# Kernel tuning notes

Hardware: AMD Instinct MI355X
Metric: run time of the kernel (lower is better)

## Reference

```python
import jax, jax.numpy as jnp
import numpy as np

N = 6000; E = 96000; DIN = 3000; FH1 = 256; FH2 = 128; GH = 128; LAT = 256
K = 10; SCALE = 9; NC = 10; AT = 0.5; ALPHA = 1.0; BN_EPS = 1e-4

# eval-mode BatchNorm1d with running_mean=0, running_var=1
def _bn(x, g, b):
    return x * (g / jnp.sqrt(1.0 + BN_EPS)) + b

def _block(x, W, bb, g, be):  # Linear + BN(eval) + ELU (dropout=identity in eval)
    return jax.nn.elu(_bn(x @ W + bb, g, be))

def _tconv(x, src, dst, Wq, Wk, Wv, Ws, bq, bk, bv, bs):
    # PyG TransformerConv, heads=1, root_weight=True, eval (no dropout)
    q = x @ Wq + bq; k = x @ Wk + bk; v = x @ Wv + bv
    sc = 1.0 / jnp.sqrt(jnp.asarray(q.shape[-1], x.dtype))
    logit = jnp.sum(q[dst] * k[src], axis=-1) * sc            # [E]
    m = jax.ops.segment_max(logit, dst, num_segments=N)
    e = jnp.exp(logit - m[dst])
    s = jax.ops.segment_sum(e, dst, num_segments=N)
    alpha = e / s[dst]                                        # softmax over incoming edges
    out = jax.ops.segment_sum(alpha[:, None] * v[src], dst, num_segments=N) + x @ Ws + bs
    return out, alpha

def _dense_adj(src, dst, alpha):
    # remove_self_loops + to_dense_adj: dense[src, dst] += alpha for src != dst
    mask = (src != dst).astype(alpha.dtype)
    return jnp.zeros((N, N), alpha.dtype).at[src, dst].add(alpha * mask)

def _encode(x, adj, adjp, ew1, eb1, eg1, ebe1, ew2, eb2, eg2, ebe2,
            cWq, cWk, cWv, cWs, cbq, cbk, cbv, cbs):
    feat = _block(_block(x, ew1, eb1, eg1, ebe1), ew2, eb2, eg2, ebe2)
    h = feat
    lastAp = None
    for l in range(3):
        o, a = _tconv(h, adj[0], adj[1], cWq[l], cWk[l], cWv[l], cWs[l], cbq[l], cbk[l], cbv[l], cbs[l])
        # middle layer applies the 'prue' conv to the freshly produced x (as in source)
        hp_in = o if l == 1 else h
        op, ap = _tconv(hp_in, adjp[0], adjp[1], cWq[l], cWk[l], cWv[l], cWs[l], cbq[l], cbk[l], cbv[l], cbs[l])
        A = _dense_adj(adj[0], adj[1], a)
        Ap = _dense_adj(adjp[0], adjp[1], ap)
        h = (1.0 - AT) * (A @ o) + AT * (Ap @ op)
        if l < 2:
            h = jax.nn.relu(h)
        lastAp = Ap
    return h, feat, lastAp

def setup_inputs():
    key = jax.random.key(0)
    ks = jax.random.split(key, 24)
    w = lambda k, sh, fan: (jax.random.normal(k, sh, jnp.float32) / np.sqrt(fan)).astype(jnp.float32)
    inp = {}
    inp['x'] = jax.random.normal(ks[0], (N, DIN), jnp.float32)
    inp['x_neighbor'] = jax.random.normal(ks[1], (N, DIN), jnp.float32)
    inp['spatial'] = jax.random.uniform(ks[2], (N, 2), jnp.float32)
    inp['adj'] = jax.random.randint(ks[3], (2, E), 0, N, dtype=jnp.int32)
    inp['adj_prue'] = jax.random.randint(ks[4], (2, E), 0, N, dtype=jnp.int32)
    # encoder
    inp['enc_W1'] = w(ks[5], (DIN, FH1), DIN); inp['enc_b1'] = jnp.zeros((FH1,))
    inp['enc_g1'] = jnp.ones((FH1,)); inp['enc_be1'] = jnp.zeros((FH1,))
    inp['enc_W2'] = w(ks[6], (FH1, FH2), FH1); inp['enc_b2'] = jnp.zeros((FH2,))
    inp['enc_g2'] = jnp.ones((FH2,)); inp['enc_be2'] = jnp.zeros((FH2,))
    # 3 TransformerConv layers (gc1, conv_hidden[0], gc2) all 128->128: stacked
    inp['conv_Wq'] = w(ks[7], (3, GH, GH), GH); inp['conv_Wk'] = w(ks[8], (3, GH, GH), GH)
    inp['conv_Wv'] = w(ks[9], (3, GH, GH), GH); inp['conv_Ws'] = w(ks[10], (3, GH, GH), GH)
    inp['conv_bq'] = jnp.zeros((3, GH)); inp['conv_bk'] = jnp.zeros((3, GH))
    inp['conv_bv'] = jnp.zeros((3, GH)); inp['conv_bs'] = jnp.zeros((3, GH))
    # decoder
    inp['dec_W'] = w(ks[11], (LAT, DIN), LAT); inp['dec_b'] = jnp.zeros((DIN,))
    inp['dec_g'] = jnp.ones((DIN,)); inp['dec_be'] = jnp.zeros((DIN,))
    inp['cluster'] = w(ks[12], (NC, LAT), LAT)
    return inp

def reference(x, x_neighbor, spatial, enc_W1, enc_b1, enc_g1, enc_be1,
              enc_W2, enc_b2, enc_g2, enc_be2,
              conv_Wq, conv_Wk, conv_Wv, conv_Ws, conv_bq, conv_bk, conv_bv, conv_bs,
              dec_W, dec_b, dec_g, dec_be, cluster, adj, adj_prue):
    enc = (enc_W1, enc_b1, enc_g1, enc_be1, enc_W2, enc_b2, enc_g2, enc_be2)
    conv = (conv_Wq, conv_Wk, conv_Wv, conv_Ws, conv_bq, conv_bk, conv_bv, conv_bs)
    mu, feat_x, atten = _encode(x, adj, adj_prue, *enc, *conv)
    mu_nb, feat_nb, _ = _encode(x_neighbor, adj, adj_prue, *enc, *conv)
    z = jnp.concatenate([feat_x, mu], axis=1)          # [N, LAT]
    z_nb = jnp.concatenate([feat_nb, mu_nb], axis=1)
    # Graph_spatial: kNN in joint feature+spatial space (dense [N,N] distances)
    df = (jnp.sum(z * z, 1)[:, None] - 2.0 * (z @ z_nb.T) + jnp.sum(z_nb * z_nb, 1)[None, :])
    ds = (jnp.sum(spatial * spatial, 1)[:, None] - 2.0 * (spatial @ spatial.T)
          + jnp.sum(spatial * spatial, 1)[None, :])
    neg_top, idx_k = jax.lax.top_k(-(df + ds), K)      # [N, K]
    score_k = jax.nn.softmax(neg_top, axis=-1)
    # GCNBlock_spatial: gather scale=9 nearest neighbor features and aggregate
    idx9 = idx_k[:, :SCALE]
    x_h = z_nb[idx9]                                   # [N, 9, LAT]
    wgt = score_k[:, :SCALE]
    wgt = wgt / jnp.sum(wgt, axis=-1, keepdims=True)
    z_out = z + jnp.einsum('nk,nkd->nd', wgt, x_h)     # x1_lr
    x1_hr = (x_h * wgt[:, :, None]).reshape(N * SCALE, LAT)
    de_feat = _block(z_out, dec_W, dec_b, dec_g, dec_be)
    # student-t cluster assignment
    d2 = jnp.sum((z_out[:, None, :] - cluster[None, :, :]) ** 2, axis=2)
    q = (1.0 / (1.0 + d2 / ALPHA)) ** ((ALPHA + 1.0) / 2.0)
    q = q / jnp.sum(q, axis=1, keepdims=True)
    return (z_out, de_feat, q, feat_x, de_feat, x1_hr, atten)
```

## Files before the change

### kernel.cpp

```cpp
#include <hip/hip_runtime.h>
#include <hip/hip_bf16.h>
#include <math.h>
#include <stdint.h>

#define NN 6000
#define NE 96000
#define KDIN 3000
#define NCAND 12
#define NTILE 47
#define TCAND (NCAND*NTILE)
#define PRE 32

#define OFF_ZOUT 0
#define OFF_DE1  1536000
#define OFF_Q    19536000
#define OFF_FEAT 19596000
#define OFF_DE2  20364000
#define OFF_X1   38364000
#define OFF_ATT  52188000

__global__ void prep_k(const float* __restrict__ W1, const float* __restrict__ W2,
                       const float* __restrict__ Wq, const float* __restrict__ Wk,
                       const float* __restrict__ Wv, const float* __restrict__ Ws,
                       const float* __restrict__ bq, const float* __restrict__ bk,
                       const float* __restrict__ bv, const float* __restrict__ bs,
                       const float* __restrict__ decW, const float* __restrict__ spat,
                       double* __restrict__ W1t, double* __restrict__ W2t,
                       double* __restrict__ Bct, float* __restrict__ Dt,
                       double* __restrict__ bcat,
                       double* __restrict__ sx64, double* __restrict__ sy64,
                       double* __restrict__ ssq64,
                       float* __restrict__ sx32, float* __restrict__ sy32)
{
  int t = blockIdx.x * 256 + threadIdx.x;
  if (t < 768000){
    int n = t / 3000, k = t % 3000;
    W1t[t] = (double)W1[(size_t)k * 256 + n]; return;
  }
  t -= 768000;
  if (t < 32768){
    int n = t / 256, k = t % 256;
    W2t[t] = (double)W2[(size_t)k * 128 + n]; return;
  }
  t -= 32768;
  if (t < 196608){
    int l = t / 65536; int rem = t % 65536;
    int n = rem / 128, k = rem % 128;
    int sel = n >> 7, nn = n & 127;
    const float* Wm = sel==0 ? Wq : sel==1 ? Wk : sel==2 ? Wv : Ws;
    Bct[t] = (double)Wm[((size_t)(l*128) + k) * 128 + nn]; return;
  }
  t -= 196608;
  if (t < 768000){
    int n = t / 256, k = t % 256;
    Dt[t] = decW[(size_t)k * 3000 + n]; return;
  }
  t -= 768000;
  if (t < 1536){
    int l = t / 512, n = t % 512;
    int sel = n >> 7, nn = n & 127;
    const float* bm = sel==0 ? bq : sel==1 ? bk : sel==2 ? bv : bs;
    bcat[t] = (double)bm[l*128 + nn]; return;
  }
  t -= 1536;
  if (t < NN){
    float sx = spat[(size_t)t*2], sy = spat[(size_t)t*2+1];
    sx64[t]=(double)sx; sy64[t]=(double)sy;
    ssq64[t]=(double)sx*(double)sx + (double)sy*(double)sy;
    sx32[t]=sx; sy32[t]=sy; return;
  }
}

__global__ void castup_k(const float* __restrict__ s, double* __restrict__ d, int n){
  int t = blockIdx.x*256 + threadIdx.x;
  if (t < n) d[t] = (double)s[t];
}

template<int EPI, typename TA>
__global__ __launch_bounds__(256)
void gemm64_k(const TA* __restrict__ A, int lda,
              const double* __restrict__ Bt, int ldb,
              int M, int K, int Ncol,
              double* __restrict__ outF, int ldc,
              const double* __restrict__ bias,
              const float* __restrict__ gam, const float* __restrict__ bet,
              double* __restrict__ outF2)
{
  __shared__ double lA[64][33];
  __shared__ double lB[64][33];
  const int tid = threadIdx.x;
  const int m0 = blockIdx.y * 64;
  const int n0 = blockIdx.x * 64;
  const int tx = tid & 15;
  const int ty = tid >> 4;

  double acc[4][4];
  #pragma unroll
  for (int i=0;i<4;i++)
    #pragma unroll
    for (int j=0;j<4;j++) acc[i][j] = 0.0;

  const int nkt = (K + 31) >> 5;
  for (int kt = 0; kt < nkt; kt++){
    const int k0 = kt << 5;
    __syncthreads();
    #pragma unroll
    for (int c=0;c<8;c++){
      int lin = tid + c*256;
      int row = lin >> 5, col = lin & 31;
      int gm = m0 + row, gk = k0 + col;
      double va = 0.0, vb = 0.0;
      if (gm < M && gk < K)        va = (double)A [(size_t)gm*lda + gk];
      if (n0+row < Ncol && gk < K) vb = Bt[(size_t)(n0+row)*ldb + gk];
      lA[row][col] = va;
      lB[row][col] = vb;
    }
    __syncthreads();
    #pragma unroll 2
    for (int kk=0; kk<32; kk++){
      double a0=lA[ty][kk], a1=lA[ty+16][kk], a2=lA[ty+32][kk], a3=lA[ty+48][kk];
      double b0=lB[tx][kk], b1=lB[tx+16][kk], b2=lB[tx+32][kk], b3=lB[tx+48][kk];
      acc[0][0]+=a0*b0; acc[0][1]+=a0*b1; acc[0][2]+=a0*b2; acc[0][3]+=a0*b3;
      acc[1][0]+=a1*b0; acc[1][1]+=a1*b1; acc[1][2]+=a1*b2; acc[1][3]+=a1*b3;
      acc[2][0]+=a2*b0; acc[2][1]+=a2*b1; acc[2][2]+=a2*b2; acc[2][3]+=a2*b3;
      acc[3][0]+=a3*b0; acc[3][1]+=a3*b1; acc[3][2]+=a3*b2; acc[3][3]+=a3*b3;
    }
  }
  #pragma unroll
  for (int j=0;j<4;j++){
    int gn = n0 + tx + 16*j;
    if (gn >= Ncol) continue;
    double bi = bias[gn];
    #pragma unroll
    for (int i=0;i<4;i++){
      int gm = m0 + ty + 16*i;
      if (gm >= M) continue;
      double v = acc[i][j] + bi;
      outF[(size_t)gm*ldc + gn] = v;
      if (outF2) outF2[(size_t)gm*ldc + gn] = v;
    }
  }
}

template<typename TA>
__global__ __launch_bounds__(256)
void gemm64s_k(const TA* __restrict__ A, int lda,
               const double* __restrict__ Bt, int ldb,
               int M, int K, int kchunk, int Ncol,
               double* __restrict__ part)
{
  __shared__ double lA[64][33];
  __shared__ double lB[64][33];
  const int tid = threadIdx.x;
  const int m0 = blockIdx.y * 64;
  const int n0 = blockIdx.x * 64;
  const int tx = tid & 15;
  const int ty = tid >> 4;
  const int kbeg = blockIdx.z * kchunk;
  const int kend = min(K, kbeg + kchunk);
  double* dst = part + (size_t)blockIdx.z * M * Ncol;

  double acc[4][4];
  #pragma unroll
  for (int i=0;i<4;i++)
    #pragma unroll
    for (int j=0;j<4;j++) acc[i][j] = 0.0;

  const int nkt = (kend - kbeg + 31) >> 5;
  for (int kt = 0; kt < nkt; kt++){
    const int k0 = kbeg + (kt << 5);
    __syncthreads();
    #pragma unroll
    for (int c=0;c<8;c++){
      int lin = tid + c*256;
      int row = lin >> 5, col = lin & 31;
      int gm = m0 + row, gk = k0 + col;
      double va = 0.0, vb = 0.0;
      if (gm < M && gk < kend)        va = (double)A [(size_t)gm*lda + gk];
      if (n0+row < Ncol && gk < kend) vb = Bt[(size_t)(n0+row)*ldb + gk];
      lA[row][col] = va;
      lB[row][col] = vb;
    }
    __syncthreads();
    #pragma unroll 2
    for (int kk=0; kk<32; kk++){
      double a0=lA[ty][kk], a1=lA[ty+16][kk], a2=lA[ty+32][kk], a3=lA[ty+48][kk];
      double b0=lB[tx][kk], b1=lB[tx+16][kk], b2=lB[tx+32][kk], b3=lB[tx+48][kk];
      acc[0][0]+=a0*b0; acc[0][1]+=a0*b1; acc[0][2]+=a0*b2; acc[0][3]+=a0*b3;
      acc[1][0]+=a1*b0; acc[1][1]+=a1*b1; acc[1][2]+=a1*b2; acc[1][3]+=a1*b3;
      acc[2][0]+=a2*b0; acc[2][1]+=a2*b1; acc[2][2]+=a2*b2; acc[2][3]+=a2*b3;
      acc[3][0]+=a3*b0; acc[3][1]+=a3*b1; acc[3][2]+=a3*b2; acc[3][3]+=a3*b3;
    }
  }
  #pragma unroll
  for (int j=0;j<4;j++){
    int gn = n0 + tx + 16*j;
    if (gn >= Ncol) continue;
    #pragma unroll
    for (int i=0;i<4;i++){
      int gm = m0 + ty + 16*i;
      if (gm >= M) continue;
      dst[(size_t)gm*Ncol + gn] = acc[i][j];
    }
  }
}

__global__ void epi64_k(const double* __restrict__ part, int nsplit, size_t pstride,
                        int M, int Ncol, const double* __restrict__ bias,
                        const float* __restrict__ gam, const float* __restrict__ bet,
                        double* __restrict__ out, int ldo)
{
  int t = blockIdx.x*256 + threadIdx.x;
  if (t >= M*Ncol) return;
  int gm = t / Ncol, gn = t - gm*Ncol;
  double v = 0.0;
  for (int s=0; s<nsplit; s++) v += part[(size_t)s*pstride + t];
  const double BNS = 0.99995000374968755261;
  v += bias[gn];
  v = v * ((double)gam[gn]*BNS) + (double)bet[gn];
  v = v > 0.0 ? v : expm1(v);
  out[(size_t)gm*ldo + gn] = v;
}

__global__ __launch_bounds__(256)
void gemm32d_k(const float* __restrict__ A, int lda,
               const float* __restrict__ Bt, int ldb,
               int M, int K, int Ncol,
               float* __restrict__ out1, int ldc,
               const float* __restrict__ bias, const float* __restrict__ gam,
               const float* __restrict__ bet, float* __restrict__ out2)
{
  __shared__ float lA[64][33];
  __shared__ float lB[64][33];
  const int tid = threadIdx.x;
  const int m0 = blockIdx.y * 64;
  const int n0 = blockIdx.x * 64;
  const int tx = tid & 15;
  const int ty = tid >> 4;

  float acc[4][4];
  #pragma unroll
  for (int i=0;i<4;i++)
    #pragma unroll
    for (int j=0;j<4;j++) acc[i][j] = 0.f;

  const int nkt = (K + 31) >> 5;
  for (int kt = 0; kt < nkt; kt++){
    const int k0 = kt << 5;
    __syncthreads();
    #pragma unroll
    for (int c=0;c<8;c++){
      int lin = tid + c*256;
      int row = lin >> 5, col = lin & 31;
      int gm = m0 + row, gk = k0 + col;
      float va = 0.f, vb = 0.f;
      if (gm < M && gk < K)        va = A [(size_t)gm*lda + gk];
      if (n0+row < Ncol && gk < K) vb = Bt[(size_t)(n0+row)*ldb + gk];
      lA[row][col] = va;
      lB[row][col] = vb;
    }
    __syncthreads();
    #pragma unroll 4
    for (int kk=0; kk<32; kk++){
      float a0=lA[ty][kk], a1=lA[ty+16][kk], a2=lA[ty+32][kk], a3=lA[ty+48][kk];
      float b0=lB[tx][kk], b1=lB[tx+16][kk], b2=lB[tx+32][kk], b3=lB[tx+48][kk];
      acc[0][0]+=a0*b0; acc[0][1]+=a0*b1; acc[0][2]+=a0*b2; acc[0][3]+=a0*b3;
      acc[1][0]+=a1*b0; acc[1][1]+=a1*b1; acc[1][2]+=a1*b2; acc[1][3]+=a1*b3;
      acc[2][0]+=a2*b0; acc[2][1]+=a2*b1; acc[2][2]+=a2*b2; acc[2][3]+=a2*b3;
      acc[3][0]+=a3*b0; acc[3][1]+=a3*b1; acc[3][2]+=a3*b2; acc[3][3]+=a3*b3;
    }
  }
  const float BNS = 0.99995000374968755f;
  #pragma unroll
  for (int j=0;j<4;j++){
    int gn = n0 + tx + 16*j;
    if (gn >= Ncol) continue;
    float bi = bias[gn];
    float gs = gam[gn]*BNS, be = bet[gn];
    #pragma unroll
    for (int i=0;i<4;i++){
      int gm = m0 + ty + 16*i;
      if (gm >= M) continue;
      float v = acc[i][j] + bi;
      v = v*gs + be; v = v > 0.f ? v : expm1f(v);
      out1[(size_t)gm*ldc + gn] = v;
      out2[(size_t)gm*ldc + gn] = v;
    }
  }
}

__global__ void csr_cnt_k(const int* __restrict__ key, int* __restrict__ cnt){
  int e = blockIdx.x*256 + threadIdx.x;
  if (e < NE) atomicAdd(&cnt[key[e]], 1);
}
__global__ __launch_bounds__(256)
void csr_scan_k(const int* __restrict__ cnt, int* __restrict__ rowptr, int* __restrict__ cursor){
  __shared__ int part[256];
  int t = threadIdx.x;
  int base = t*24;
  int loc[24]; int s=0;
  #pragma unroll
  for (int u=0;u<24;u++){
    int idx = base+u;
    int v = (idx<NN) ? cnt[idx] : 0;
    loc[u] = s; s += v;
  }
  part[t] = s;
  __syncthreads();
  if (t==0){
    int run=0;
    for (int u=0;u<256;u++){ int tmp=part[u]; part[u]=run; run+=tmp; }
  }
  __syncthreads();
  int off = part[t];
  #pragma unroll
  for (int u=0;u<24;u++){
    int idx = base+u;
    if (idx<NN){ rowptr[idx]=off+loc[u]; cursor[idx]=off+loc[u]; }
  }
  if (t==255) rowptr[NN] = off + s;
}
__global__ void csr_fill_k(const int* __restrict__ key, int* __restrict__ cursor,
                           int* __restrict__ elist){
  int e = blockIdx.x*256 + threadIdx.x;
  if (e < NE){ int pos = atomicAdd(&cursor[key[e]], 1); elist[pos] = e; }
}

__global__ __launch_bounds__(256)
void attn_k(double* __restrict__ QKVS, const int* __restrict__ rowptr,
            const int* __restrict__ elist, const int* __restrict__ src,
            double* __restrict__ alpha)
{
  __shared__ double lg[4][128];
  const int w = threadIdx.x >> 6;
  const int node = blockIdx.x*4 + w;
  if (node >= NN) return;
  const int lane = threadIdx.x & 63;
  const int e0 = rowptr[node], e1 = rowptr[node+1];
  const int deg = e1 - e0;
  if (deg <= 0) return;
  const double SC = 0.088388347648318447;
  const double* q = QKVS + (size_t)node*512;
  double q0 = q[lane], q1 = q[lane+64];

  if (deg <= 128){
    double m = -1.0e300;
    for (int i=0;i<deg;i++){
      const double* k = QKVS + (size_t)src[elist[e0+i]]*512 + 128;
      double p = q0*k[lane] + q1*k[lane+64];
      #pragma unroll
      for (int off=32; off; off>>=1) p += __shfl_xor(p, off);
      p *= SC;
      if (lane==0) lg[w][i] = p;
      m = fmax(m, p);
    }
    double S = 0.0;
    for (int i=0;i<deg;i++){
      double ex = exp(lg[w][i] - m);
      if (lane==0) lg[w][i] = ex;
      S += ex;
    }
    double inv = 1.0 / S;
    double o0 = QKVS[(size_t)node*512 + 384 + lane];
    double o1 = QKVS[(size_t)node*512 + 448 + lane];
    for (int i=0;i<deg;i++){
      int e = elist[e0+i];
      double a = lg[w][i] * inv;
      const double* v = QKVS + (size_t)src[e]*512 + 256;
      o0 = fma(a, v[lane],    o0);
      o1 = fma(a, v[lane+64], o1);
      if (lane==0) alpha[e] = a;
    }
    QKVS[(size_t)node*512 + 384 + lane] = o0;
    QKVS[(size_t)node*512 + 448 + lane] = o1;
  } else {
    double m = -1.0e300;
    for (int i=0;i<deg;i++){
      const double* k = QKVS + (size_t)src[elist[e0+i]]*512 + 128;
      double p = q0*k[lane] + q1*k[lane+64];
      #pragma unroll
      for (int off=32; off; off>>=1) p += __shfl_xor(p, off);
      m = fmax(m, p*SC);
    }
    double S = 0.0;
    for (int i=0;i<deg;i++){
      const double* k = QKVS + (size_t)src[elist[e0+i]]*512 + 128;
      double p = q0*k[lane] + q1*k[lane+64];
      #pragma unroll
      for (int off=32; off; off>>=1) p += __shfl_xor(p, off);
      S += exp(p*SC - m);
    }
    double inv = 1.0 / S;
    double o0 = QKVS[(size_t)node*512 + 384 + lane];
    double o1 = QKVS[(size_t)node*512 + 448 + lane];
    for (int i=0;i<deg;i++){
      int e = elist[e0+i];
      const double* k = QKVS + (size_t)src[e]*512 + 128;
      double p = q0*k[lane] + q1*k[lane+64];
      #pragma unroll
      for (int off=32; off; off>>=1) p += __shfl_xor(p, off);
      double a = exp(p*SC - m) * inv;
      const double* v = QKVS + (size_t)src[e]*512 + 256;
      o0 = fma(a, v[lane],    o0);
      o1 = fma(a, v[lane+64], o1);
      if (lane==0) alpha[e] = a;
    }
    QKVS[(size_t)node*512 + 384 + lane] = o0;
    QKVS[(size_t)node*512 + 448 + lane] = o1;
  }
}

__global__ __launch_bounds__(256)
void spmm_csr_k(const double* __restrict__ QK1, const double* __restrict__ QK2,
                const int* __restrict__ rpSA, const int* __restrict__ elSA,
                const int* __restrict__ dstA, const double* __restrict__ aA,
                const int* __restrict__ rpSP, const int* __restrict__ elSP,
                const int* __restrict__ dstP, const double* __restrict__ aP,
                double* __restrict__ out, int ldo, int offo, int dorelu)
{
  const int node = blockIdx.x*4 + (threadIdx.x>>6);
  if (node >= NN) return;
  const int lane = threadIdx.x & 63;
  double a0 = 0.0, a1 = 0.0;
  for (int idx = rpSA[node]; idx < rpSA[node+1]; ++idx){
    int e = elSA[idx]; int d = dstA[e];
    if (d != node){
      double wgt = 0.5 * aA[e];
      const double* o = QK1 + (size_t)d*512 + 384;
      a0 = fma(wgt, o[lane],    a0);
      a1 = fma(wgt, o[lane+64], a1);
    }
  }
  for (int idx = rpSP[node]; idx < rpSP[node+1]; ++idx){
    int e = elSP[idx]; int d = dstP[e];
    if (d != node){
      double wgt = 0.5 * aP[e];
      const double* o = QK2 + (size_t)d*512 + 384;
      a0 = fma(wgt, o[lane],    a0);
      a1 = fma(wgt, o[lane+64], a1);
    }
  }
  if (dorelu){ a0 = fmax(a0, 0.0); a1 = fmax(a1, 0.0); }
  out[(size_t)node*ldo + offo + lane]      = a0;
  out[(size_t)node*ldo + offo + 64 + lane] = a1;
}

__global__ void att_scatter_k(const int* __restrict__ src, const int* __restrict__ dst,
                              const double* __restrict__ alpha, float* __restrict__ att)
{
  int e = blockIdx.x*256 + threadIdx.x;
  if (e >= NE) return;
  int s = src[e], d = dst[e];
  if (s == d) return;
  atomicAdd(&att[(size_t)s*NN + d], (float)alpha[e]);
}

__global__ __launch_bounds__(256)
void dist32_k(const float* __restrict__ Z, const float* __restrict__ Znb,
              const float* __restrict__ sxA, const float* __restrict__ syA, const float* __restrict__ cjA,
              float* __restrict__ candV, int* __restrict__ candI)
{
  __shared__ __align__(16) char smem[33024 + 1536];
  float (*lA)[36]    = (float(*)[36])(smem);
  float (*lB)[36]    = (float(*)[36])(smem + 9216);
  float (*stile)[129]= (float(*)[129])(smem);
  float* sSx = (float*)(smem + 33024);
  float* sSy = sSx + 128;
  float* sC  = sSy + 128;

  const int tid = threadIdx.x;
  const int m0 = blockIdx.y * 64;
  const int n0 = blockIdx.x * 128;
  const int tx = tid & 15;
  const int ty = tid >> 4;

  if (tid < 128){
    int jg = n0 + tid;
    if (jg < NN){ sSx[tid]=sxA[jg]; sSy[tid]=syA[jg]; sC[tid]=cjA[jg]; }
    else        { sSx[tid]=0.f; sSy[tid]=0.f; sC[tid]=-3e38f; }
  }

  float acc[4][8];
  #pragma unroll
  for (int i=0;i<4;i++)
    #pragma unroll
    for (int j=0;j<8;j++) acc[i][j] = 0.f;

  for (int kt = 0; kt < 8; kt++){
    const int k0 = kt << 5;
    __syncthreads();
    #pragma unroll
    for (int c=0;c<2;c++){
      int lin = tid + c*256;
      int row = lin >> 3, c4 = (lin & 7) << 2;
      int gm = m0 + row;
      float4 v = make_float4(0.f,0.f,0.f,0.f);
      if (gm < NN) v = *(const float4*)(Z + (size_t)gm*256 + k0 + c4);
      *(float4*)&lA[row][c4] = v;
    }
    #pragma unroll
    for (int c=0;c<4;c++){
      int lin = tid + c*256;
      int row = lin >> 3, c4 = (lin & 7) << 2;
      int gn = n0 + row;
      float4 v = make_float4(0.f,0.f,0.f,0.f);
      if (gn < NN) v = *(const float4*)(Znb + (size_t)gn*256 + k0 + c4);
      *(float4*)&lB[row][c4] = v;
    }
    __syncthreads();
    #pragma unroll 2
    for (int kk=0; kk<32; kk+=4){
      float4 a[4], b[8];
      #pragma unroll
      for (int i=0;i<4;i++) a[i] = *(const float4*)&lA[ty+16*i][kk];
      #pragma unroll
      for (int j=0;j<8;j++) b[j] = *(const float4*)&lB[tx+16*j][kk];
      #pragma unroll
      for (int u=0;u<4;u++){
        #pragma unroll
        for (int i=0;i<4;i++){
          float av = (&a[i].x)[u];
          #pragma unroll
          for (int j=0;j<8;j++)
            acc[i][j] += av * (&b[j].x)[u];
        }
      }
    }
  }

  __syncthreads();
  #pragma unroll
  for (int i=0;i<4;i++)
    #pragma unroll
    for (int j=0;j<8;j++)
      stile[ty+16*i][tx+16*j] = acc[i][j];
  __syncthreads();

  if (tid < 64){
    const int gi = m0 + tid;
    if (gi < NN){
      float sxi = sxA[gi], syi = syA[gi];
      float tv[NCAND]; int ti[NCAND];
      #pragma unroll
      for (int p=0;p<NCAND;p++){ tv[p] = -3.4e38f; ti[p] = -1; }
      #pragma unroll 1
      for (int jj=0; jj<128; jj++){
        float s = 2.f*stile[tid][jj] + 2.f*(sxi*sSx[jj] + syi*sSy[jj]) + sC[jj];
        if (s > tv[NCAND-1]){
          bool g[NCAND];
          #pragma unroll
          for (int p=0;p<NCAND;p++) g[p] = s > tv[p];
          #pragma unroll
          for (int p=NCAND-1;p>0;--p) if (g[p-1]){ tv[p]=tv[p-1]; ti[p]=ti[p-1]; }
          #pragma unroll
          for (int p=0;p<NCAND;p++){ bool pl = g[p] && (p==0 || !g[p-1]); if (pl){ tv[p]=s; ti[p]=n0+jj; } }
        }
      }
      size_t base = ((size_t)gi*NTILE + blockIdx.x)*NCAND;
      #pragma unroll
      for (int p=0;p<NCAND;p++){ candV[base+p]=tv[p]; candI[base+p]=ti[p]; }
    }
  }
}

__global__ __launch_bounds__(256)
void merge64_k(const float* __restrict__ candV, const int* __restrict__ candI,
               const double* __restrict__ Z, const double* __restrict__ Znb,
               const double* __restrict__ sx64, const double* __restrict__ sy64,
               double* __restrict__ wgt9, int* __restrict__ idx9)
{
  __shared__ double zi[256];
  __shared__ int    fjS[TCAND];
  __shared__ float  wbv[4];
  __shared__ int    wbc[4];
  __shared__ int    chosen;
  __shared__ int    pj[PRE];
  __shared__ double ps[PRE];

  const int i = blockIdx.x;
  const int t = threadIdx.x;
  const int lane = t & 63, wv = t >> 6;

  zi[t] = Z[(size_t)i*256 + t];

  float v0 = -3.4e38f, v1 = -3.4e38f, v2 = -3.4e38f;
  const int c0 = t, c1 = t + 256, c2 = t + 512;
  {
    float vv = candV[(size_t)i*TCAND + c0];
    int jj = candI[(size_t)i*TCAND + c0];
    fjS[c0] = jj;
    if (jj >= 0) v0 = vv;
  }
  if (c1 < TCAND){
    float vv = candV[(size_t)i*TCAND + c1];
    int jj = candI[(size_t)i*TCAND + c1];
    fjS[c1] = jj;
    if (jj >= 0) v1 = vv;
  }
  if (c2 < TCAND){
    float vv = candV[(size_t)i*TCAND + c2];
    int jj = candI[(size_t)i*TCAND + c2];
    fjS[c2] = jj;
    if (jj >= 0) v2 = vv;
  }
  __syncthreads();

  for (int it = 0; it < PRE; it++){
    float bv = v0; int bc = c0;
    if (v1 > bv || (v1 == bv && c1 < bc)){ bv = v1; bc = c1; }
    if (v2 > bv || (v2 == bv && c2 < bc)){ bv = v2; bc = c2; }
    #pragma unroll
    for (int off = 32; off; off >>= 1){
      float ov = __shfl_xor(bv, off);
      int   oc = __shfl_xor(bc, off);
      if (ov > bv || (ov == bv && oc < bc)){ bv = ov; bc = oc; }
    }
    if (lane == 0){ wbv[wv] = bv; wbc[wv] = bc; }
    __syncthreads();
    if (t == 0){
      float gb = wbv[0]; int gc = wbc[0];
      #pragma unroll
      for (int w2 = 1; w2 < 4; w2++)
        if (wbv[w2] > gb || (wbv[w2] == gb && wbc[w2] < gc)){ gb = wbv[w2]; gc = wbc[w2]; }
      chosen = gc;
      pj[it] = fjS[gc];
    }
    __syncthreads();
    int gc = chosen;
    if (c0 == gc) v0 = -3.4e38f;
    if (c1 == gc) v1 = -3.4e38f;
    if (c2 == gc) v2 = -3.4e38f;
  }

  const double sxi = sx64[i], syi = sy64[i];
  for (int c = wv; c < PRE; c += 4){
    int j = pj[c];
    const double* zj = Znb + (size_t)j*256;
    double p = 0.0;
    #pragma unroll
    for (int u = 0; u < 4; u++){
      double b = zj[lane + 64*u];
      double a = zi[lane + 64*u];
      p = fma(2.0*a - b, b, p);
    }
    #pragma unroll
    for (int off = 32; off; off >>= 1) p += __shfl_xor(p, off);
    double sxj = sx64[j], syj = sy64[j];
    double s = p + 2.0*(sxi*sxj + syi*syj) - (sxj*sxj + syj*syj);
    if (lane == 0) ps[c] = s;
  }
  __syncthreads();

  if (t == 0){
    double tv9[9]; int ti9[9];
    #pragma unroll
    for (int p = 0; p < 9; p++){ tv9[p] = -1.0e301; ti9[p] = 0x7FFFFFFF; }
    for (int c = 0; c < PRE; c++){
      double s = ps[c]; int j = pj[c];
      if (!((s > tv9[8]) || (s == tv9[8] && j < ti9[8]))) continue;
      int p = 8;
      while (p > 0 && ((s > tv9[p-1]) || (s == tv9[p-1] && j < ti9[p-1]))){
        tv9[p] = tv9[p-1]; ti9[p] = ti9[p-1]; --p;
      }
      tv9[p] = s; ti9[p] = j;
    }
    double m = tv9[0], e[9], S = 0.0;
    #pragma unroll
    for (int k = 0; k < 9; k++){ e[k] = exp(tv9[k] - m); S += e[k]; }
    #pragma unroll
    for (int k = 0; k < 9; k++){
      wgt9[(size_t)i*9 + k] = e[k] / S;
      idx9[(size_t)i*9 + k] = ti9[k];
    }
  }
}

__global__ __launch_bounds__(256)
void znbprep_k(const double* __restrict__ znb, const double* __restrict__ ssq64,
               float* __restrict__ cjA)
{
  __shared__ double red[256];
  int i = blockIdx.x, d = threadIdx.x;
  double v = znb[(size_t)i*256 + d];
  red[d] = v*v;
  __syncthreads();
  for (int s=128; s; s>>=1){ if (d<s) red[d]+=red[d+s]; __syncthreads(); }
  if (d==0) cjA[i] = -(float)(red[0] + ssq64[i]);
}
__global__ void castz_k(const double* __restrict__ z64, float* __restrict__ z32, int n){
  int t = blockIdx.x*256+threadIdx.x;
  if (t < n) z32[t] = (float)z64[t];
}
__global__ void featout_k(const double* __restrict__ z, float* __restrict__ o){
  int t = blockIdx.x*256+threadIdx.x;
  if (t < NN*128){ int i=t>>7, d=t&127; o[t] = (float)z[(size_t)i*256 + d]; }
}

__global__ __launch_bounds__(256)
void zout_k(const double* __restrict__ Z, const double* __restrict__ Znb,
            const int* __restrict__ idx9, const double* __restrict__ wgt9,
            float* __restrict__ zoOut, float* __restrict__ zoF32, float* __restrict__ x1)
{
  int i = blockIdx.x; int d = threadIdx.x;
  double a = Z[(size_t)i*256 + d];
  #pragma unroll
  for (int k=0;k<9;k++){
    int j = idx9[(size_t)i*9+k];
    double w = wgt9[(size_t)i*9+k];
    double t = w * Znb[(size_t)j*256 + d];
    a += t;
    x1[((size_t)i*9+k)*256 + d] = (float)t;
  }
  float af = (float)a;
  zoOut[(size_t)i*256+d] = af;
  zoF32[(size_t)i*256+d] = af;
}

__global__ __launch_bounds__(256)
void q_k(const float* __restrict__ zoF, const float* __restrict__ clus, float* __restrict__ qB)
{
  __shared__ float wred[10][4];
  __shared__ float qs[10];
  int i = blockIdx.x, d = threadIdx.x;
  int lane = d & 63, wv = d >> 6;
  float zo = zoF[(size_t)i*256 + d];
  #pragma unroll
  for (int c=0;c<10;c++){
    float df = zo - clus[(size_t)c*256 + d];
    float p = df*df;
    #pragma unroll
    for (int off=32; off; off>>=1) p += __shfl_down(p, off);
    if (lane == 0) wred[c][wv] = p;
  }
  __syncthreads();
  if (d < 10){
    float d2 = wred[d][0]+wred[d][1]+wred[d][2]+wred[d][3];
    qs[d] = 1.f/(1.f + d2);
  }
  __syncthreads();
  if (d < 10){
    float s = 0.f;
    #pragma unroll
    for (int c=0;c<10;c++) s += qs[c];
    qB[(size_t)i*10 + d] = qs[d]/s;
  }
}

extern "C" void kernel_launch(void* const* d_in, const int* in_sizes, int n_in,
                              void* d_out, int out_size, void* d_ws, size_t ws_size,
                              hipStream_t stream)
{
  (void)in_sizes; (void)n_in; (void)out_size; (void)ws_size;
  const float* x    = (const float*)d_in[0];
  const float* xnb  = (const float*)d_in[1];
  const float* spat = (const float*)d_in[2];
  const int*   adj  = (const int*)d_in[3];
  const int*   adjp = (const int*)d_in[4];
  const float* W1   = (const float*)d_in[5];
  const float* b1   = (const float*)d_in[6];
  const float* g1   = (const float*)d_in[7];
  const float* be1  = (const float*)d_in[8];
  const float* W2   = (const float*)d_in[9];
  const float* b2   = (const float*)d_in[10];
  const float* g2   = (const float*)d_in[11];
  const float* be2  = (const float*)d_in[12];
  const float* Wq   = (const float*)d_in[13];
  const float* Wk   = (const float*)d_in[14];
  const float* Wv   = (const float*)d_in[15];
  const float* Wsm  = (const float*)d_in[16];
  const float* bq   = (const float*)d_in[17];
  const float* bk   = (const float*)d_in[18];
  const float* bv   = (const float*)d_in[19];
  const float* bs   = (const float*)d_in[20];
  const float* decW = (const float*)d_in[21];
  const float* decb = (const float*)d_in[22];
  const float* decg = (const float*)d_in[23];
  const float* decbe= (const float*)d_in[24];
  const float* clus = (const float*)d_in[25];
  float* outF = (float*)d_out;
  const int* srcA = adj,  *dstA = adj + NE;
  const int* srcP = adjp, *dstP = adjp + NE;

  char* wsb = (char*)d_ws;
  size_t off = 0;
  auto alloc = [&](size_t bytes)->char*{
    char* p = wsb + off;
    off = (off + bytes + 255) & ~(size_t)255;
    return p;
  };
  double* W1t  = (double*)alloc(768000*8);
  double* W2t  = (double*)alloc(32768*8);
  double* Bct  = (double*)alloc(196608*8);
  float*  Dt   = (float*) alloc(768000*4);
  double* bcat = (double*)alloc(1536*8);
  double* sx64 = (double*)alloc(NN*8);
  double* sy64 = (double*)alloc(NN*8);
  double* ssq64= (double*)alloc(NN*8);
  float*  sx32 = (float*) alloc(NN*4);
  float*  sy32 = (float*) alloc(NN*4);
  double* b1c  = (double*)alloc(256*8);
  double* b2c  = (double*)alloc(128*8);
  double* H1   = (double*)alloc((size_t)NN*256*8);
  double* zX64 = (double*)alloc((size_t)NN*256*8);
  double* zNB64= (double*)alloc((size_t)NN*256*8);
  double* hcur = (double*)alloc((size_t)NN*128*8);
  double* QK1  = (double*)alloc((size_t)NN*512*8);
  double* QK2  = (double*)alloc((size_t)NN*512*8);
  double* alphaA=(double*)alloc((size_t)NE*8);
  double* alphaP=(double*)alloc((size_t)NE*8);
  double* part = (double*)alloc((size_t)4*NN*256*8);
  int* rpDA = (int*)alloc((NN+1)*4);
  int* rpDP = (int*)alloc((NN+1)*4);
  int* rpSA = (int*)alloc((NN+1)*4);
  int* rpSP = (int*)alloc((NN+1)*4);
  int* curDA= (int*)alloc(NN*4);
  int* curDP= (int*)alloc(NN*4);
  int* curSA= (int*)alloc(NN*4);
  int* curSP= (int*)alloc(NN*4);
  int* elDA = (int*)alloc(NE*4);
  int* elDP = (int*)alloc(NE*4);
  int* elSA = (int*)alloc(NE*4);
  int* elSP = (int*)alloc(NE*4);
  float*  zX32 = (float*) alloc((size_t)NN*256*4);
  float*  zNB32= (float*) alloc((size_t)NN*256*4);
  float*  cjA  = (float*) alloc(NN*4);
  float*  candV= (float*) alloc((size_t)NN*TCAND*4);
  int*    candI= (int*)   alloc((size_t)NN*TCAND*4);
  int*    idx9 = (int*)   alloc((size_t)NN*9*4);
  double* wgt9 = (double*)alloc((size_t)NN*9*8);
  float*  zoF32= (float*) alloc((size_t)NN*256*4);

  prep_k<<<6926, 256, 0, stream>>>(W1, W2, Wq, Wk, Wv, Wsm, bq, bk, bv, bs, decW, spat,
                                   W1t, W2t, Bct, Dt, bcat,
                                   sx64, sy64, ssq64, sx32, sy32);
  castup_k<<<1, 256, 0, stream>>>(b1, b1c, 256);
  castup_k<<<1, 256, 0, stream>>>(b2, b2c, 128);

  hipMemsetAsync(curDA, 0, NN*4, stream);
  hipMemsetAsync(curDP, 0, NN*4, stream);
  hipMemsetAsync(curSA, 0, NN*4, stream);
  hipMemsetAsync(curSP, 0, NN*4, stream);
  csr_cnt_k<<<375, 256, 0, stream>>>(dstA, curDA);
  csr_cnt_k<<<375, 256, 0, stream>>>(dstP, curDP);
  csr_cnt_k<<<375, 256, 0, stream>>>(srcA, curSA);
  csr_cnt_k<<<375, 256, 0, stream>>>(srcP, curSP);
  csr_scan_k<<<1, 256, 0, stream>>>(curDA, rpDA, curDA);
  csr_scan_k<<<1, 256, 0, stream>>>(curDP, rpDP, curDP);
  csr_scan_k<<<1, 256, 0, stream>>>(curSA, rpSA, curSA);
  csr_scan_k<<<1, 256, 0, stream>>>(curSP, rpSP, curSP);
  csr_fill_k<<<375, 256, 0, stream>>>(dstA, curDA, elDA);
  csr_fill_k<<<375, 256, 0, stream>>>(dstP, curDP, elDP);
  csr_fill_k<<<375, 256, 0, stream>>>(srcA, curSA, elSA);
  csr_fill_k<<<375, 256, 0, stream>>>(srcP, curSP, elSP);

  auto enc = [&](const float* xin, double* zbuf, bool isX){
    gemm64s_k<float><<<dim3(4,94,4), 256, 0, stream>>>(xin, KDIN, W1t, KDIN,
                                                       NN, KDIN, 768, 256, part);
    epi64_k<<<(NN*256+255)/256, 256, 0, stream>>>(part, 4, (size_t)NN*256,
                                                  NN, 256, b1c, g1, be1, H1, 256);
    gemm64s_k<double><<<dim3(2,94,4), 256, 0, stream>>>(H1, 256, W2t, 256,
                                                        NN, 256, 64, 128, part);
    epi64_k<<<(NN*128+255)/256, 256, 0, stream>>>(part, 4, (size_t)NN*128,
                                                  NN, 128, b2c, g2, be2, zbuf, 256);
    const double* hin = zbuf; int ldh = 256;
    for (int l=0; l<3; l++){
      const double* Bh = Bct + (size_t)l*65536;
      const double* bc = bcat + l*512;
      if (l != 1){
        gemm64_k<0,double><<<dim3(8,94), 256, 0, stream>>>(hin, ldh, Bh, 128, NN, 128, 512,
                                                           QK1, 512, bc, nullptr, nullptr, QK2);
        attn_k<<<1500, 256, 0, stream>>>(QK1, rpDA, elDA, srcA, alphaA);
        attn_k<<<1500, 256, 0, stream>>>(QK2, rpDP, elDP, srcP, alphaP);
      } else {
        gemm64_k<0,double><<<dim3(8,94), 256, 0, stream>>>(hin, ldh, Bh, 128, NN, 128, 512,
                                                           QK1, 512, bc, nullptr, nullptr, nullptr);
        attn_k<<<1500, 256, 0, stream>>>(QK1, rpDA, elDA, srcA, alphaA);
        gemm64_k<0,double><<<dim3(8,94), 256, 0, stream>>>(QK1 + 384, 512, Bh, 128, NN, 128, 512,
                                                           QK2, 512, bc, nullptr, nullptr, nullptr);
        attn_k<<<1500, 256, 0, stream>>>(QK2, rpDP, elDP, srcP, alphaP);
      }
      if (isX && l == 2){
        hipMemsetAsync(outF + (size_t)OFF_ATT, 0, (size_t)NN*NN*4, stream);
        att_scatter_k<<<375, 256, 0, stream>>>(srcP, dstP, alphaP, outF + (size_t)OFF_ATT);
      }
      if (l < 2){
        spmm_csr_k<<<1500, 256, 0, stream>>>(QK1, QK2, rpSA, elSA, dstA, alphaA,
                                             rpSP, elSP, dstP, alphaP, hcur, 128, 0, 1);
        hin = hcur; ldh = 128;
      } else {
        spmm_csr_k<<<1500, 256, 0, stream>>>(QK1, QK2, rpSA, elSA, dstA, alphaA,
                                             rpSP, elSP, dstP, alphaP, zbuf, 256, 128, 0);
      }
    }
  };
  enc(x,   zX64,  true);
  enc(xnb, zNB64, false);

  castz_k<<<6000, 256, 0, stream>>>(zX64,  zX32,  NN*256);
  castz_k<<<6000, 256, 0, stream>>>(zNB64, zNB32, NN*256);
  znbprep_k<<<NN, 256, 0, stream>>>(zNB64, ssq64, cjA);
  dist32_k<<<dim3(NTILE,94), 256, 0, stream>>>(zX32, zNB32, sx32, sy32, cjA, candV, candI);
  merge64_k<<<NN, 256, 0, stream>>>(candV, candI, zX64, zNB64, sx64, sy64, wgt9, idx9);

  zout_k<<<NN, 256, 0, stream>>>(zX64, zNB64, idx9, wgt9,
                                 outF + (size_t)OFF_ZOUT, zoF32, outF + (size_t)OFF_X1);
  gemm32d_k<<<dim3(47,94), 256, 0, stream>>>(zoF32, 256, Dt, 256, NN, 256, 3000,
                                             outF + (size_t)OFF_DE1, 3000, decb, decg, decbe,
                                             outF + (size_t)OFF_DE2);
  q_k<<<NN, 256, 0, stream>>>(zoF32, clus, outF + (size_t)OFF_Q);
  featout_k<<<3000, 256, 0, stream>>>(zX64, outF + (size_t)OFF_FEAT);
}
```

Before: 3.229 ms.

## Compute kNN distance tile with split-bf16 MFMA instead of FP32 FMA

Z and Z_nb are each split into high and low bf16 parts, and the pairwise dot products for the kNN candidate search are computed with three bf16 MFMA products (hh, hl, lh) accumulating into fp32. The block tile grows from 64x128 to 128x128, and the candidate scan runs in two 64-column halves over a smaller shared stage. The aim is to replace the scalar FP32 FMA GEMM with matrix-core throughput while keeping near-fp32 accuracy for candidate selection, since the final merge re-ranks in double. The cost is lower precision in candidate ordering, with some risk of missing a true neighbour, plus an extra split pass.

```diff
diff --git a/kernel.cpp b/kernel.cpp
--- a/kernel.cpp
+++ b/kernel.cpp
@@ -18,6 +18,18 @@
 #define OFF_DE2  20364000
 #define OFF_X1   38364000
 #define OFF_ATT  52188000
+
+typedef __attribute__((ext_vector_type(8))) short short8;
+typedef __attribute__((ext_vector_type(4))) float f32x4;
+
+__device__ __forceinline__ unsigned short f2bf(float f){
+  unsigned int u = __float_as_uint(f);
+  u += 0x7FFFu + ((u >> 16) & 1u);
+  return (unsigned short)(u >> 16);
+}
+__device__ __forceinline__ float bf2f(unsigned short h){
+  return __uint_as_float(((unsigned int)h) << 16);
+}
 
 __global__ void prep_k(const float* __restrict__ W1, const float* __restrict__ W2,
                        const float* __restrict__ Wq, const float* __restrict__ Wk,
@@ -74,6 +86,17 @@
 __global__ void castup_k(const float* __restrict__ s, double* __restrict__ d, int n){
   int t = blockIdx.x*256 + threadIdx.x;
   if (t < n) d[t] = (double)s[t];
+}
+
+__global__ void splitz_k(const double* __restrict__ z64, unsigned short* __restrict__ zh,
+                         unsigned short* __restrict__ zl, int n){
+  int t = blockIdx.x*256 + threadIdx.x;
+  if (t < n){
+    float v = (float)z64[t];
+    unsigned short h = f2bf(v);
+    float r = v - bf2f(h);
+    zh[t] = h; zl[t] = f2bf(r);
+  }
 }
 
 template<int EPI, typename TA>
@@ -456,23 +479,31 @@
 }
 
 __global__ __launch_bounds__(256)
-void dist32_k(const float* __restrict__ Z, const float* __restrict__ Znb,
-              const float* __restrict__ sxA, const float* __restrict__ syA, const float* __restrict__ cjA,
+void distmf_k(const unsigned short* __restrict__ zXh, const unsigned short* __restrict__ zXl,
+              const unsigned short* __restrict__ zNh, const unsigned short* __restrict__ zNl,
+              const float* __restrict__ sxA, const float* __restrict__ syA,
+              const float* __restrict__ cjA,
               float* __restrict__ candV, int* __restrict__ candI)
 {
-  __shared__ __align__(16) char smem[33024 + 1536];
-  float (*lA)[36]    = (float(*)[36])(smem);
-  float (*lB)[36]    = (float(*)[36])(smem + 9216);
-  float (*stile)[129]= (float(*)[129])(smem);
-  float* sSx = (float*)(smem + 33024);
+  __shared__ __align__(16) char smem[40960 + 1536];
+  typedef unsigned short u16;
+  u16 (*lAh)[40] = (u16(*)[40])(smem);
+  u16 (*lAl)[40] = (u16(*)[40])(smem + 10240);
+  u16 (*lBh)[40] = (u16(*)[40])(smem + 20480);
+  u16 (*lBl)[40] = (u16(*)[40])(smem + 30720);
+  float (*stile)[67] = (float(*)[67])(smem);
+  float* sSx = (float*)(smem + 40960);
   float* sSy = sSx + 128;
   float* sC  = sSy + 128;
 
   const int tid = threadIdx.x;
-  const int m0 = blockIdx.y * 64;
+  const int m0 = blockIdx.y * 128;
   const int n0 = blockIdx.x * 128;
-  const int tx = tid & 15;
-  const int ty = tid >> 4;
+  const int lane = tid & 63;
+  const int wave = tid >> 6;
+  const int wm = wave >> 1, wn = wave & 1;
+  const int lr = lane & 15;
+  const int lk = (lane >> 4) * 8;
 
   if (tid < 128){
     int jg = n0 + tid;
@@ -480,72 +511,83 @@
     else        { sSx[tid]=0.f; sSy[tid]=0.f; sC[tid]=-3e38f; }
   }
 
-  float acc[4][8];
+  f32x4 acc[4][4];
   #pragma unroll
   for (int i=0;i<4;i++)
     #pragma unroll
-    for (int j=0;j<8;j++) acc[i][j] = 0.f;
+    for (int j=0;j<4;j++) acc[i][j] = (f32x4){0.f,0.f,0.f,0.f};
 
   for (int kt = 0; kt < 8; kt++){
     const int k0 = kt << 5;
     __syncthreads();
     #pragma unroll
-    for (int c=0;c<2;c++){
-      int lin = tid + c*256;
-      int row = lin >> 3, c4 = (lin & 7) << 2;
-      int gm = m0 + row;
-      float4 v = make_float4(0.f,0.f,0.f,0.f);
-      if (gm < NN) v = *(const float4*)(Z + (size_t)gm*256 + k0 + c4);
-      *(float4*)&lA[row][c4] = v;
-    }
-    #pragma unroll
     for (int c=0;c<4;c++){
       int lin = tid + c*256;
-      int row = lin >> 3, c4 = (lin & 7) << 2;
-      int gn = n0 + row;
-      float4 v = make_float4(0.f,0.f,0.f,0.f);
-      if (gn < NN) v = *(const float4*)(Znb + (size_t)gn*256 + k0 + c4);
-      *(float4*)&lB[row][c4] = v;
-    }
-    __syncthreads();
-    #pragma unroll 2
-    for (int kk=0; kk<32; kk+=4){
-      float4 a[4], b[8];
+      int row = lin >> 3;
+      int kc = (lin & 7) << 2;
+      int gm = m0 + row, gn = n0 + row;
+      ushort4 vh = {0,0,0,0}, vl = {0,0,0,0}, wh = {0,0,0,0}, wl = {0,0,0,0};
+      if (gm < NN){
+        vh = *(const ushort4*)(zXh + (size_t)gm*256 + k0 + kc);
+        vl = *(const ushort4*)(zXl + (size_t)gm*256 + k0 + kc);
+      }
+      if (gn < NN){
+        wh = *(const ushort4*)(zNh + (size_t)gn*256 + k0 + kc);
+        wl = *(const ushort4*)(zNl + (size_t)gn*256 + k0 + kc);
+      }
+      *(ushort4*)&lAh[row][kc] = vh;
+      *(ushort4*)&lAl[row][kc] = vl;
+      *(ushort4*)&lBh[row][kc] = wh;
+      *(ushort4*)&lBl[row][kc] = wl;
+    }
+    __syncthreads();
+    short8 ah[4], al[4];
+    #pragma unroll
+    for (int fm=0; fm<4; fm++){
+      ah[fm] = *(const short8*)&lAh[wm*64 + fm*16 + lr][lk];
+      al[fm] = *(const short8*)&lAl[wm*64 + fm*16 + lr][lk];
+    }
+    #pragma unroll
+    for (int fn=0; fn<4; fn++){
+      short8 bh = *(const short8*)&lBh[wn*64 + fn*16 + lr][lk];
+      short8 bl = *(const short8*)&lBl[wn*64 + fn*16 + lr][lk];
       #pragma unroll
-      for (int i=0;i<4;i++) a[i] = *(const float4*)&lA[ty+16*i][kk];
+      for (int fm=0; fm<4; fm++){
+        acc[fm][fn] = __builtin_amdgcn_mfma_f32_16x16x32_bf16(ah[fm], bh, acc[fm][fn], 0,0,0);
+        acc[fm][fn] = __builtin_amdgcn_mfma_f32_16x16x32_bf16(ah[fm], bl, acc[fm][fn], 0,0,0);
+        acc[fm][fn] = __builtin_amdgcn_mfma_f32_16x16x32_bf16(al[fm], bh, acc[fm][fn], 0,0,0);
+      }
+    }
+  }
+
+  float tv[NCAND]; int ti[NCAND];
+  #pragma unroll
+  for (int p=0;p<NCAND;p++){ tv[p] = -3.4e38f; ti[p] = -1; }
+  const int gi = m0 + tid;
+  float sxi = 0.f, syi = 0.f;
+  if (tid < 128 && gi < NN){ sxi = sxA[gi]; syi = syA[gi]; }
+
+  for (int jh = 0; jh < 2; jh++){
+    __syncthreads();
+    if (wn == jh){
       #pragma unroll
-      for (int j=0;j<8;j++) b[j] = *(const float4*)&lB[tx+16*j][kk];
-      #pragma unroll
-      for (int u=0;u<4;u++){
+      for (int fm=0;fm<4;fm++){
         #pragma unroll
-        for (int i=0;i<4;i++){
-          float av = (&a[i].x)[u];
+        for (int fn=0;fn<4;fn++){
+          int lrow = wm*64 + fm*16 + ((lane>>4)<<2);
+          int lcol = fn*16 + lr;
           #pragma unroll
-          for (int j=0;j<8;j++)
-            acc[i][j] += av * (&b[j].x)[u];
+          for (int r=0;r<4;r++)
+            stile[lrow + r][lcol] = acc[fm][fn][r];
         }
       }
     }
-  }
-
-  __syncthreads();
-  #pragma unroll
-  for (int i=0;i<4;i++)
-    #pragma unroll
-    for (int j=0;j<8;j++)
-      stile[ty+16*i][tx+16*j] = acc[i][j];
-  __syncthreads();
-
-  if (tid < 64){
-    const int gi = m0 + tid;
-    if (gi < NN){
-      float sxi = sxA[gi], syi = syA[gi];
-      float tv[NCAND]; int ti[NCAND];
-      #pragma unroll
-      for (int p=0;p<NCAND;p++){ tv[p] = -3.4e38f; ti[p] = -1; }
+    __syncthreads();
+    if (tid < 128 && gi < NN){
       #pragma unroll 1
-      for (int jj=0; jj<128; jj++){
-        float s = 2.f*stile[tid][jj] + 2.f*(sxi*sSx[jj] + syi*sSy[jj]) + sC[jj];
+      for (int jj=0; jj<64; jj++){
+        int j = jh*64 + jj;
+        float s = 2.f*stile[tid][jj] + 2.f*(sxi*sSx[j] + syi*sSy[j]) + sC[j];
         if (s > tv[NCAND-1]){
           bool g[NCAND];
           #pragma unroll
@@ -553,13 +595,15 @@
           #pragma unroll
           for (int p=NCAND-1;p>0;--p) if (g[p-1]){ tv[p]=tv[p-1]; ti[p]=ti[p-1]; }
           #pragma unroll
-          for (int p=0;p<NCAND;p++){ bool pl = g[p] && (p==0 || !g[p-1]); if (pl){ tv[p]=s; ti[p]=n0+jj; } }
+          for (int p=0;p<NCAND;p++){ bool pl = g[p] && (p==0 || !g[p-1]); if (pl){ tv[p]=s; ti[p]=n0+j; } }
         }
       }
-      size_t base = ((size_t)gi*NTILE + blockIdx.x)*NCAND;
-      #pragma unroll
-      for (int p=0;p<NCAND;p++){ candV[base+p]=tv[p]; candI[base+p]=ti[p]; }
-    }
+    }
+  }
+  if (tid < 128 && gi < NN){
+    size_t base = ((size_t)gi*NTILE + blockIdx.x)*NCAND;
+    #pragma unroll
+    for (int p=0;p<NCAND;p++){ candV[base+p]=tv[p]; candI[base+p]=ti[p]; }
   }
 }
 
@@ -686,10 +730,6 @@
   __syncthreads();
   for (int s=128; s; s>>=1){ if (d<s) red[d]+=red[d+s]; __syncthreads(); }
   if (d==0) cjA[i] = -(float)(red[0] + ssq64[i]);
-}
-__global__ void castz_k(const double* __restrict__ z64, float* __restrict__ z32, int n){
-  int t = blockIdx.x*256+threadIdx.x;
-  if (t < n) z32[t] = (float)z64[t];
 }
 __global__ void featout_k(const double* __restrict__ z, float* __restrict__ o){
   int t = blockIdx.x*256+threadIdx.x;
@@ -821,8 +861,10 @@
   int* elDP = (int*)alloc(NE*4);
   int* elSA = (int*)alloc(NE*4);
   int* elSP = (int*)alloc(NE*4);
-  float*  zX32 = (float*) alloc((size_t)NN*256*4);
-  float*  zNB32= (float*) alloc((size_t)NN*256*4);
+  unsigned short* zXh = (unsigned short*)alloc((size_t)NN*256*2);
+  unsigned short* zXl = (unsigned short*)alloc((size_t)NN*256*2);
+  unsigned short* zNh = (unsigned short*)alloc((size_t)NN*256*2);
+  unsigned short* zNl = (unsigned short*)alloc((size_t)NN*256*2);
   float*  cjA  = (float*) alloc(NN*4);
   float*  candV= (float*) alloc((size_t)NN*TCAND*4);
   int*    candI= (int*)   alloc((size_t)NN*TCAND*4);
@@ -896,10 +938,11 @@
   enc(x,   zX64,  true);
   enc(xnb, zNB64, false);
 
-  castz_k<<<6000, 256, 0, stream>>>(zX64,  zX32,  NN*256);
-  castz_k<<<6000, 256, 0, stream>>>(zNB64, zNB32, NN*256);
+  splitz_k<<<6000, 256, 0, stream>>>(zX64,  zXh, zXl, NN*256);
+  splitz_k<<<6000, 256, 0, stream>>>(zNB64, zNh, zNl, NN*256);
   znbprep_k<<<NN, 256, 0, stream>>>(zNB64, ssq64, cjA);
-  dist32_k<<<dim3(NTILE,94), 256, 0, stream>>>(zX32, zNB32, sx32, sy32, cjA, candV, candI);
+  distmf_k<<<dim3(NTILE,47), 256, 0, stream>>>(zXh, zXl, zNh, zNl,
+                                               sx32, sy32, cjA, candV, candI);
   merge64_k<<<NN, 256, 0, stream>>>(candV, candI, zX64, zNB64, sx64, sy64, wgt9, idx9);
 
   zout_k<<<NN, 256, 0, stream>>>(zX64, zNB64, idx9, wgt9,
```

Result: faster. 2.982 ms (-7.6%).
